# Kernel optimization log

Hardware: AMD Instinct MI355X
Metric: run time of the kernel (lower is better)

Reference implementation:

```python
import jax, jax.numpy as jnp
import numpy as np
from math import sqrt

DIM = 256
NUM_HEADS = 4
GROUPS = 32  # min(256//4, 32)
EPS = 1e-6


def group_norm(x, gamma, beta, groups=GROUPS, eps=EPS):
    # x: (B, C, H, W); normalize per group over (C//G, H, W)
    B, C, H, W = x.shape
    xg = x.reshape(B, groups, C // groups, H, W)
    mu = jnp.mean(xg, axis=(2, 3, 4), keepdims=True)
    var = jnp.var(xg, axis=(2, 3, 4), keepdims=True)
    xn = ((xg - mu) * jax.lax.rsqrt(var + eps)).reshape(B, C, H, W)
    return xn * gamma[None, :, None, None] + beta[None, :, None, None]


def lin_on_channel(x, W, bias):
    # torch Linear on channel dim: W is (out, in)
    return jnp.einsum('bchw,oc->bohw', x, W) + bias[None, :, None, None]


def setup_inputs() -> dict:
    key = jax.random.key(0)
    ks = jax.random.split(key, 14)
    B, C, H, W = 16, DIM, 32, 32
    s = 1.0 / sqrt(DIM)
    return {
        'a': jax.random.normal(ks[0], (B, C, H, W), jnp.float32),
        'b': jax.random.normal(ks[1], (B, C, H, W), jnp.float32),
        'Wq': jax.random.normal(ks[2], (DIM, DIM), jnp.float32) * s,
        'bq': jnp.zeros((DIM,), jnp.float32),
        'Wk': jax.random.normal(ks[3], (DIM, DIM), jnp.float32) * s,
        'bk': jnp.zeros((DIM,), jnp.float32),
        'Wv': jax.random.normal(ks[4], (DIM, DIM), jnp.float32) * s,
        'bv': jnp.zeros((DIM,), jnp.float32),
        'Wp': jax.random.normal(ks[5], (DIM, DIM), jnp.float32) * s,
        'bp': jnp.zeros((DIM,), jnp.float32),
        'gnA_w': jnp.ones((DIM,), jnp.float32),
        'gnA_b': jnp.zeros((DIM,), jnp.float32),
        'gnB_w': jnp.ones((DIM,), jnp.float32),
        'gnB_b': jnp.zeros((DIM,), jnp.float32),
    }


def reference(a, b, Wq, bq, Wk, bk, Wv, bv, Wp, bp, gnA_w, gnA_b, gnB_w, gnB_b):
    B, C, H, W = a.shape
    _, _, H2, W2 = b.shape
    dh = DIM // NUM_HEADS
    skip_b = b
    an = group_norm(a, gnA_w, gnA_b)
    bn = group_norm(b, gnB_w, gnB_b)
    q = lin_on_channel(bn, Wq, bq).reshape(B, NUM_HEADS, dh, H2, W2)
    k = lin_on_channel(an, Wk, bk).reshape(B, NUM_HEADS, dh, H, W)
    # NOTE: value uses pre-posemb but post-groupnorm 'a' (same as an here)
    v = lin_on_channel(an, Wv, bv).reshape(B, NUM_HEADS, dh, H, W)
    scores = jnp.einsum('bhdxy,bhdij->bhxyij', q, k) / sqrt(DIM)
    attn = jax.nn.softmax(scores.reshape(B, NUM_HEADS, H2, W2, H * W), axis=-1)
    attn = attn.reshape(B, NUM_HEADS, H2, W2, H, W)
    h = jnp.einsum('bhxyij,bhdij->bhdxy', attn, v).reshape(B, DIM, H2, W2)
    h = lin_on_channel(h, Wp, bp)
    ret = skip_b + h
    return ret / sqrt(2.0)
```

## Files before the change

kernel.cpp:

```cpp
#include <hip/hip_runtime.h>
#include <hip/hip_bf16.h>

#define BSZ 16
#define CDIM 256
#define NPIX 1024
#define NH 4
#define DHD 64
#define EPSV 1e-6f
#define QSCALE 0.0625f
#define INV_SQRT2 0.70710678118654752440f

typedef __attribute__((ext_vector_type(4))) float f32x4;
typedef __attribute__((ext_vector_type(8))) __bf16 bf16x8;
typedef __attribute__((ext_vector_type(4))) __bf16 bf16x4;

#define ASYNC16(gp, lp) __builtin_amdgcn_global_load_lds( \
    (const __attribute__((address_space(1))) void*)(gp),  \
    (__attribute__((address_space(3))) void*)(lp), 16, 0, 0)

#define OFF_WBF   0UL
#define OFF_STATS (512UL*1024)
#define OFF_ANT   (1024UL*1024)
#define OFF_BNT   (OFF_ANT + 8UL*1024*1024)
#define OFF_Q     (OFF_BNT + 8UL*1024*1024)
#define OFF_K     (OFF_Q   + 8UL*1024*1024)
#define OFF_V     (OFF_K   + 8UL*1024*1024)
#define OFF_H     (OFF_V   + 8UL*1024*1024)

__global__ __launch_bounds__(256) void prep_w(const float* __restrict__ Wq, const float* __restrict__ Wk,
                                              const float* __restrict__ Wv, const float* __restrict__ Wp,
                                              __bf16* __restrict__ out){
  int m = blockIdx.y;
  const float* src = (m==0)?Wq:(m==1)?Wk:(m==2)?Wv:Wp;
  float scale = (m==0)?QSCALE:1.0f;
  int idx = (blockIdx.x*256 + threadIdx.x)*4;
  float4 v = *(const float4*)(src + idx);
  bf16x4 o;
  o[0]=(__bf16)(v.x*scale); o[1]=(__bf16)(v.y*scale);
  o[2]=(__bf16)(v.z*scale); o[3]=(__bf16)(v.w*scale);
  *(bf16x4*)(out + m*65536 + idx) = o;
}

__global__ __launch_bounds__(256) void gn_stats(const float* __restrict__ xa, const float* __restrict__ xb,
                                                float2* __restrict__ stats){
  int bx = blockIdx.x;
  int t = bx >> 9; int rem = bx & 511; int bb = rem >> 5; int g = rem & 31;
  const float* src = (t ? xb : xa) + ((size_t)(bb*CDIM + g*8))*NPIX;
  float s = 0.f, ss = 0.f;
  for (int i = 0; i < 8; i++){
    float4 v = *(const float4*)(src + (threadIdx.x + 256*i)*4);
    s  += v.x+v.y+v.z+v.w;
    ss += v.x*v.x+v.y*v.y+v.z*v.z+v.w*v.w;
  }
  __shared__ float rs[256], rss[256];
  rs[threadIdx.x]=s; rss[threadIdx.x]=ss; __syncthreads();
  for (int st=128; st>0; st>>=1){
    if (threadIdx.x < st){ rs[threadIdx.x]+=rs[threadIdx.x+st]; rss[threadIdx.x]+=rss[threadIdx.x+st]; }
    __syncthreads();
  }
  if (threadIdx.x==0){
    float mean = rs[0]*(1.0f/8192.0f);
    float var  = rss[0]*(1.0f/8192.0f) - mean*mean;
    stats[(t*16+bb)*32+g] = make_float2(mean, rsqrtf(var + EPSV));
  }
}

__global__ __launch_bounds__(256) void norm_t(const float* __restrict__ xa, const float* __restrict__ xb,
                                              const float* __restrict__ gAw, const float* __restrict__ gAb,
                                              const float* __restrict__ gBw, const float* __restrict__ gBb,
                                              const float2* __restrict__ stats,
                                              __bf16* __restrict__ ant, __bf16* __restrict__ bnt){
  __shared__ __align__(16) __bf16 T[64][72];
  int t = blockIdx.z;
  const float* src = t ? xb : xa;
  const float* gw  = t ? gBw : gAw;
  const float* gb  = t ? gBb : gAb;
  __bf16* dst = t ? bnt : ant;
  int bb = blockIdx.y >> 2, cblk = blockIdx.y & 3;
  int p0 = blockIdx.x*64, c0 = cblk*64;
  int tid = threadIdx.x;
  int r16 = tid>>4, c4 = tid&15;
  for (int pass=0; pass<4; pass++){
    int cl = r16 + 16*pass;
    int c  = c0 + cl;
    float2 ms = stats[(t*16+bb)*32 + (c>>3)];
    float sc  = ms.y * gw[c];
    float off = gb[c] - ms.x*sc;
    float4 v = *(const float4*)(src + ((size_t)(bb*CDIM + c))*NPIX + p0 + c4*4);
    T[c4*4+0][cl] = (__bf16)(v.x*sc+off);
    T[c4*4+1][cl] = (__bf16)(v.y*sc+off);
    T[c4*4+2][cl] = (__bf16)(v.z*sc+off);
    T[c4*4+3][cl] = (__bf16)(v.w*sc+off);
  }
  __syncthreads();
  for (int pass=0; pass<2; pass++){
    int slot = tid + 256*pass;
    int pl = slot>>3, ch = slot&7;
    *(float4*)(dst + ((size_t)(bb*NPIX + p0 + pl))*CDIM + c0 + ch*8) = *(float4*)&T[pl][ch*8];
  }
}

__global__ __launch_bounds__(256,2) void gemm_qk(const __bf16* __restrict__ Wqk,
    const __bf16* __restrict__ bnt, const __bf16* __restrict__ ant,
    const float* __restrict__ bq, const float* __restrict__ bk,
    __bf16* __restrict__ qws, __bf16* __restrict__ kws){
  __shared__ __align__(16) __bf16 As[128][76], Bs[128][76];
  int i0 = blockIdx.x;
  int wg = (i0&7)*64 + (i0>>3);
  int my = wg&3, nx = wg>>2;
  int m0 = my*128, n0 = nx*128;
  const __bf16* Bm = (my<2) ? bnt : ant;
  int tid=threadIdx.x, lane=tid&63, wid=tid>>6;
  int wm=(wid>>1)*64, wn=(wid&1)*64, g=lane>>4, c=lane&15;
  f32x4 acc[4][4];
  #pragma unroll
  for (int i=0;i<4;i++)
    #pragma unroll
    for (int j=0;j<4;j++) acc[i][j]=(f32x4){0.f,0.f,0.f,0.f};
  int row[4], ch[4];
  #pragma unroll
  for (int i=0;i<4;i++){ int slot=tid+256*i; row[i]=slot>>3; ch[i]=slot&7; }
  for (int k0=0; k0<256; k0+=64){
    #pragma unroll
    for (int i=0;i<4;i++){
      *(float4*)&As[row[i]][ch[i]*8] = *(const float4*)(Wqk + (size_t)(m0+row[i])*256 + k0 + ch[i]*8);
      *(float4*)&Bs[row[i]][ch[i]*8] = *(const float4*)(Bm  + (size_t)(n0+row[i])*256 + k0 + ch[i]*8);
    }
    __syncthreads();
    #pragma unroll
    for (int ks=0;ks<2;ks++){
      bf16x8 af[4], bfr[4];
      #pragma unroll
      for (int i=0;i<4;i++) af[i]  = *(bf16x8*)&As[wm+i*16+c][ks*32+g*8];
      #pragma unroll
      for (int j=0;j<4;j++) bfr[j] = *(bf16x8*)&Bs[wn+j*16+c][ks*32+g*8];
      #pragma unroll
      for (int i=0;i<4;i++)
        #pragma unroll
        for (int j=0;j<4;j++)
          acc[i][j] = __builtin_amdgcn_mfma_f32_16x16x32_bf16(af[i], bfr[j], acc[i][j],0,0,0);
    }
    __syncthreads();
  }
  const float* bias = (my<2)? bq : bk;
  float bscale = (my<2)? QSCALE : 1.0f;
  __bf16* dst = (my<2)? qws : kws;
  int mbase = (my<2)? m0 : (m0-256);
  #pragma unroll
  for (int fm=0;fm<4;fm++){
    #pragma unroll
    for (int fn=0;fn<4;fn++){
      int o = mbase + wm + fm*16 + g*4;
      int n = n0 + wn + fn*16 + c;
      int bb=n>>10, p=n&1023;
      f32x4 v = acc[fm][fn];
      bf16x4 pk;
      #pragma unroll
      for (int r=0;r<4;r++) pk[r] = (__bf16)(v[r] + bias[o+r]*bscale);
      *(bf16x4*)(dst + ((size_t)((bb*4+(o>>6))*1024 + p))*64 + (o&63)) = pk;
    }
  }
}

__global__ __launch_bounds__(256,2) void gemm_sw(const __bf16* __restrict__ A,
    const __bf16* __restrict__ Wn, const float* __restrict__ bias,
    void* __restrict__ dst_, const float* __restrict__ skip, int mode){
  __shared__ __align__(16) __bf16 As[128][76], Bs[64][76];
  int i0 = blockIdx.x;
  int wg = (i0&7)*64 + (i0>>3);
  int ny = wg&3, mx = wg>>2;
  int m0 = mx*128, n0 = ny*64;
  int tid=threadIdx.x, lane=tid&63, wid=tid>>6;
  int wm=(wid>>1)*64, wn=(wid&1)*32, g=lane>>4, c=lane&15;
  f32x4 acc[4][2];
  #pragma unroll
  for (int i=0;i<4;i++)
    #pragma unroll
    for (int j=0;j<2;j++) acc[i][j]=(f32x4){0.f,0.f,0.f,0.f};
  int rowA[4], chA[4], rowB[2], chB[2];
  #pragma unroll
  for (int i=0;i<4;i++){ int slot=tid+256*i; rowA[i]=slot>>3; chA[i]=slot&7; }
  #pragma unroll
  for (int i=0;i<2;i++){ int slot=tid+256*i; rowB[i]=slot>>3; chB[i]=slot&7; }
  for (int k0=0; k0<256; k0+=64){
    #pragma unroll
    for (int i=0;i<4;i++)
      *(float4*)&As[rowA[i]][chA[i]*8] = *(const float4*)(A  + (size_t)(m0+rowA[i])*256 + k0 + chA[i]*8);
    #pragma unroll
    for (int i=0;i<2;i++)
      *(float4*)&Bs[rowB[i]][chB[i]*8] = *(const float4*)(Wn + (size_t)(n0+rowB[i])*256 + k0 + chB[i]*8);
    __syncthreads();
    #pragma unroll
    for (int ks=0;ks<2;ks++){
      bf16x8 af[4], bfr[2];
      #pragma unroll
      for (int i=0;i<4;i++) af[i]  = *(bf16x8*)&As[wm+i*16+c][ks*32+g*8];
      #pragma unroll
      for (int j=0;j<2;j++) bfr[j] = *(bf16x8*)&Bs[wn+j*16+c][ks*32+g*8];
      #pragma unroll
      for (int i=0;i<4;i++)
        #pragma unroll
        for (int j=0;j<2;j++)
          acc[i][j] = __builtin_amdgcn_mfma_f32_16x16x32_bf16(af[i], bfr[j], acc[i][j],0,0,0);
    }
    __syncthreads();
  }
  #pragma unroll
  for (int fm=0;fm<4;fm++){
    #pragma unroll
    for (int fn=0;fn<2;fn++){
      int m = m0 + wm + fm*16 + g*4;
      int n = n0 + wn + fn*16 + c;
      int bb=m>>10, p=m&1023;
      f32x4 v = acc[fm][fn];
      if (mode==0){
        float bv = bias[n];
        bf16x4 pk;
        #pragma unroll
        for (int r=0;r<4;r++) pk[r] = (__bf16)(v[r] + bv);
        *(bf16x4*)((__bf16*)dst_ + ((size_t)((bb*4+(n>>6))*64 + (n&63)))*1024 + p) = pk;
      } else {
        float bv = bias[n];
        size_t addr = (size_t)(bb*256 + n)*1024 + p;
        float4 sk = *(const float4*)(skip + addr);
        float4 ov;
        ov.x=(sk.x+v[0]+bv)*INV_SQRT2; ov.y=(sk.y+v[1]+bv)*INV_SQRT2;
        ov.z=(sk.z+v[2]+bv)*INV_SQRT2; ov.w=(sk.w+v[3]+bv)*INV_SQRT2;
        *(float4*)((float*)dst_ + addr) = ov;
      }
    }
  }
}

__global__ __launch_bounds__(256,4) void attn_k(const __bf16* __restrict__ q, const __bf16* __restrict__ k,
                                                const __bf16* __restrict__ v, __bf16* __restrict__ hout){
  __shared__ __align__(16) __bf16 Kb[2][4096];
  __shared__ __align__(16) __bf16 Vb[2][4096];
  __shared__ __align__(16) __bf16 Pl[4][1024];
  int i0 = blockIdx.x;
  int wg = (i0&7)*128 + (i0>>3);
  int bh = wg>>4, qblk = wg&15;
  int tid = threadIdx.x, lane = tid&63, w = tid>>6;
  int g = lane>>4, c = lane&15;
  int bb = bh>>2, h = bh&3;
  const char* kbyte = (const char*)(k + (size_t)bh*NPIX*DHD);
  const char* vbyte = (const char*)(v + (size_t)bh*DHD*NPIX);
  const __bf16* qbase = q + (size_t)bh*NPIX*DHD;

  int qrow = qblk*64 + w*16 + c;
  bf16x8 qf0 = *(const bf16x8*)(qbase + (size_t)qrow*64 +      g*8);
  bf16x8 qf1 = *(const bf16x8*)(qbase + (size_t)qrow*64 + 32 + g*8);

  int srow = w*8 + (lane>>3);
  int scol = ((lane&7) ^ (lane>>3)) << 4;
  const char* ks0 = kbyte + srow*128 + scol;
  const char* vs0 = vbyte + (size_t)srow*2048 + scol;

  f32x4 oacc[4];
  #pragma unroll
  for (int i=0;i<4;i++) oacc[i] = (f32x4){0.f,0.f,0.f,0.f};
  float la0=0.f, la1=0.f, la2=0.f, la3=0.f;
  int cs = (c&7)<<4;
  char* pw = (char*)&Pl[w][0];

  #define STAGE(buf, kt) { \
    const char* ks_ = ks0 + (size_t)(kt)*8192; \
    const char* vs_ = vs0 + (size_t)(kt)*128; \
    ASYNC16(ks_,          &Kb[buf][w*512]); \
    ASYNC16(ks_ + 4096,   &Kb[buf][2048 + w*512]); \
    ASYNC16(vs_,          &Vb[buf][w*512]); \
    ASYNC16(vs_ + 65536,  &Vb[buf][2048 + w*512]); }

  STAGE(0, 0)
  for (int kt=0; kt<16; kt++){
    int cur = kt&1;
    __syncthreads();
    if (kt<15) STAGE(cur^1, kt+1)
    const char* KL = (const char*)&Kb[cur][0];
    const char* VL = (const char*)&Vb[cur][0];
    f32x4 s[4];
    #pragma unroll
    for (int fn=0; fn<4; fn++){
      int r = fn*16+c;
      bf16x8 kb0 = *(const bf16x8*)(KL + r*128 + ((     g*16) ^ cs));
      bf16x8 kb1 = *(const bf16x8*)(KL + r*128 + ((64 + g*16) ^ cs));
      f32x4 z = (f32x4){0.f,0.f,0.f,0.f};
      z     = __builtin_amdgcn_mfma_f32_16x16x32_bf16(qf0, kb0, z, 0,0,0);
      s[fn] = __builtin_amdgcn_mfma_f32_16x16x32_bf16(qf1, kb1, z, 0,0,0);
    }
    #pragma unroll
    for (int fn=0; fn<4; fn++){
      int cb = (fn*16+c)*2;
      float p0 = __expf(s[fn][0]); la0 += p0;
      float p1 = __expf(s[fn][1]); la1 += p1;
      float p2 = __expf(s[fn][2]); la2 += p2;
      float p3 = __expf(s[fn][3]); la3 += p3;
      *(__bf16*)(pw + (g*4+0)*128 + (cb ^ (((g*4+0)&7)<<4))) = (__bf16)p0;
      *(__bf16*)(pw + (g*4+1)*128 + (cb ^ (((g*4+1)&7)<<4))) = (__bf16)p1;
      *(__bf16*)(pw + (g*4+2)*128 + (cb ^ (((g*4+2)&7)<<4))) = (__bf16)p2;
      *(__bf16*)(pw + (g*4+3)*128 + (cb ^ (((g*4+3)&7)<<4))) = (__bf16)p3;
    }
    bf16x8 pb0 = *(const bf16x8*)(pw + c*128 + ((     g*16) ^ cs));
    bf16x8 pb1 = *(const bf16x8*)(pw + c*128 + ((64 + g*16) ^ cs));
    #pragma unroll
    for (int fm=0; fm<4; fm++){
      int r = fm*16+c;
      bf16x8 va0 = *(const bf16x8*)(VL + r*128 + ((     g*16) ^ cs));
      bf16x8 va1 = *(const bf16x8*)(VL + r*128 + ((64 + g*16) ^ cs));
      oacc[fm] = __builtin_amdgcn_mfma_f32_16x16x32_bf16(va0, pb0, oacc[fm], 0,0,0);
      oacc[fm] = __builtin_amdgcn_mfma_f32_16x16x32_bf16(va1, pb1, oacc[fm], 0,0,0);
    }
  }
  #undef STAGE

  la0 += __shfl_xor(la0,1); la0 += __shfl_xor(la0,2); la0 += __shfl_xor(la0,4); la0 += __shfl_xor(la0,8);
  la1 += __shfl_xor(la1,1); la1 += __shfl_xor(la1,2); la1 += __shfl_xor(la1,4); la1 += __shfl_xor(la1,8);
  la2 += __shfl_xor(la2,1); la2 += __shfl_xor(la2,2); la2 += __shfl_xor(la2,4); la2 += __shfl_xor(la2,8);
  la3 += __shfl_xor(la3,1); la3 += __shfl_xor(la3,2); la3 += __shfl_xor(la3,4); la3 += __shfl_xor(la3,8);
  float vsel = ((c&3)==0)? la0 : ((c&3)==1)? la1 : ((c&3)==2)? la2 : la3;
  float lq = __shfl(vsel, (c>>2)*16 + (c&3));
  float linv = 1.0f / lq;

  int qg = qblk*64 + w*16 + c;
  #pragma unroll
  for (int fm=0; fm<4; fm++){
    bf16x4 pk;
    #pragma unroll
    for (int r=0;r<4;r++) pk[r] = (__bf16)(oacc[fm][r]*linv);
    *(bf16x4*)(hout + ((size_t)(bb*NPIX + qg))*CDIM + h*64 + fm*16 + g*4) = pk;
  }
}

extern "C" void kernel_launch(void* const* d_in, const int* in_sizes, int n_in,
                              void* d_out, int out_size, void* d_ws, size_t ws_size,
                              hipStream_t stream) {
  const float* xa  = (const float*)d_in[0];
  const float* xb  = (const float*)d_in[1];
  const float* Wq  = (const float*)d_in[2];
  const float* bq  = (const float*)d_in[3];
  const float* Wk  = (const float*)d_in[4];
  const float* bk  = (const float*)d_in[5];
  const float* Wv  = (const float*)d_in[6];
  const float* bv  = (const float*)d_in[7];
  const float* Wp  = (const float*)d_in[8];
  const float* bp  = (const float*)d_in[9];
  const float* gAw = (const float*)d_in[10];
  const float* gAb = (const float*)d_in[11];
  const float* gBw = (const float*)d_in[12];
  const float* gBb = (const float*)d_in[13];

  char* ws = (char*)d_ws;
  __bf16* wbf   = (__bf16*)(ws + OFF_WBF);
  float2* stats = (float2*)(ws + OFF_STATS);
  __bf16* ant   = (__bf16*)(ws + OFF_ANT);
  __bf16* bnt   = (__bf16*)(ws + OFF_BNT);
  __bf16* qws   = (__bf16*)(ws + OFF_Q);
  __bf16* kws   = (__bf16*)(ws + OFF_K);
  __bf16* vws   = (__bf16*)(ws + OFF_V);
  __bf16* hws   = (__bf16*)(ws + OFF_H);

  prep_w<<<dim3(64,4), 256, 0, stream>>>(Wq, Wk, Wv, Wp, wbf);
  gn_stats<<<1024, 256, 0, stream>>>(xa, xb, stats);
  norm_t<<<dim3(16,64,2), 256, 0, stream>>>(xa, xb, gAw, gAb, gBw, gBb, stats, ant, bnt);
  gemm_qk<<<512, 256, 0, stream>>>(wbf, bnt, ant, bq, bk, qws, kws);
  gemm_sw<<<512, 256, 0, stream>>>(ant, wbf + 2*65536, bv, vws, nullptr, 0);
  attn_k<<<1024, 256, 0, stream>>>(qws, kws, vws, hws);
  gemm_sw<<<512, 256, 0, stream>>>(hws, wbf + 3*65536, bp, d_out, xb, 1);
}
```

Measured before the change: 174.5 us.

## Fuse group-norm stats with normalize-transpose and merge QK and V projection launches

```diff
diff --git a/kernel.cpp b/kernel.cpp
--- a/kernel.cpp
+++ b/kernel.cpp
@@ -41,123 +41,167 @@
   *(bf16x4*)(out + m*65536 + idx) = o;
 }
 
-__global__ __launch_bounds__(256) void gn_stats(const float* __restrict__ xa, const float* __restrict__ xb,
-                                                float2* __restrict__ stats){
+__global__ __launch_bounds__(256) void gn_fused(const float* __restrict__ xa, const float* __restrict__ xb,
+    const float* __restrict__ gAw, const float* __restrict__ gAb,
+    const float* __restrict__ gBw, const float* __restrict__ gBb,
+    __bf16* __restrict__ ant, __bf16* __restrict__ bnt){
+  __shared__ float S[8192];
+  __shared__ float red[8];
   int bx = blockIdx.x;
-  int t = bx >> 9; int rem = bx & 511; int bb = rem >> 5; int g = rem & 31;
-  const float* src = (t ? xb : xa) + ((size_t)(bb*CDIM + g*8))*NPIX;
-  float s = 0.f, ss = 0.f;
-  for (int i = 0; i < 8; i++){
-    float4 v = *(const float4*)(src + (threadIdx.x + 256*i)*4);
+  int t = bx>>9, rem = bx&511, b = rem>>5, g = rem&31;
+  const float* src = (t ? xb : xa) + ((size_t)(b*CDIM + g*8))*NPIX;
+  const float* gw  = t ? gBw : gAw;
+  const float* gb  = t ? gBb : gAb;
+  __bf16* dst = (t ? bnt : ant) + (size_t)b*NPIX*CDIM + g*8;
+  int tid = threadIdx.x, lane = tid&63, w = tid>>6;
+  float s=0.f, ss=0.f;
+  #pragma unroll
+  for (int k=0;k<8;k++){
+    int flat = tid + 256*k;
+    float4 v = *(const float4*)(src + (size_t)flat*4);
+    *(float4*)&S[flat*4] = v;
     s  += v.x+v.y+v.z+v.w;
     ss += v.x*v.x+v.y*v.y+v.z*v.z+v.w*v.w;
   }
-  __shared__ float rs[256], rss[256];
-  rs[threadIdx.x]=s; rss[threadIdx.x]=ss; __syncthreads();
-  for (int st=128; st>0; st>>=1){
-    if (threadIdx.x < st){ rs[threadIdx.x]+=rs[threadIdx.x+st]; rss[threadIdx.x]+=rss[threadIdx.x+st]; }
-    __syncthreads();
-  }
-  if (threadIdx.x==0){
-    float mean = rs[0]*(1.0f/8192.0f);
-    float var  = rss[0]*(1.0f/8192.0f) - mean*mean;
-    stats[(t*16+bb)*32+g] = make_float2(mean, rsqrtf(var + EPSV));
-  }
-}
-
-__global__ __launch_bounds__(256) void norm_t(const float* __restrict__ xa, const float* __restrict__ xb,
-                                              const float* __restrict__ gAw, const float* __restrict__ gAb,
-                                              const float* __restrict__ gBw, const float* __restrict__ gBb,
-                                              const float2* __restrict__ stats,
-                                              __bf16* __restrict__ ant, __bf16* __restrict__ bnt){
-  __shared__ __align__(16) __bf16 T[64][72];
-  int t = blockIdx.z;
-  const float* src = t ? xb : xa;
-  const float* gw  = t ? gBw : gAw;
-  const float* gb  = t ? gBb : gAb;
-  __bf16* dst = t ? bnt : ant;
-  int bb = blockIdx.y >> 2, cblk = blockIdx.y & 3;
-  int p0 = blockIdx.x*64, c0 = cblk*64;
-  int tid = threadIdx.x;
-  int r16 = tid>>4, c4 = tid&15;
-  for (int pass=0; pass<4; pass++){
-    int cl = r16 + 16*pass;
-    int c  = c0 + cl;
-    float2 ms = stats[(t*16+bb)*32 + (c>>3)];
-    float sc  = ms.y * gw[c];
-    float off = gb[c] - ms.x*sc;
-    float4 v = *(const float4*)(src + ((size_t)(bb*CDIM + c))*NPIX + p0 + c4*4);
-    T[c4*4+0][cl] = (__bf16)(v.x*sc+off);
-    T[c4*4+1][cl] = (__bf16)(v.y*sc+off);
-    T[c4*4+2][cl] = (__bf16)(v.z*sc+off);
-    T[c4*4+3][cl] = (__bf16)(v.w*sc+off);
-  }
+  #pragma unroll
+  for (int m=32;m>0;m>>=1){ s += __shfl_xor(s,m); ss += __shfl_xor(ss,m); }
+  if (lane==0){ red[w]=s; red[4+w]=ss; }
   __syncthreads();
-  for (int pass=0; pass<2; pass++){
-    int slot = tid + 256*pass;
-    int pl = slot>>3, ch = slot&7;
-    *(float4*)(dst + ((size_t)(bb*NPIX + p0 + pl))*CDIM + c0 + ch*8) = *(float4*)&T[pl][ch*8];
-  }
-}
-
-__global__ __launch_bounds__(256,2) void gemm_qk(const __bf16* __restrict__ Wqk,
+  float st  = red[0]+red[1]+red[2]+red[3];
+  float sst = red[4]+red[5]+red[6]+red[7];
+  float mean = st*(1.0f/8192.0f);
+  float var  = sst*(1.0f/8192.0f) - mean*mean;
+  float rstd = rsqrtf(var + EPSV);
+  float sc[8], off[8];
+  #pragma unroll
+  for (int c2=0;c2<8;c2++){ sc[c2]=rstd*gw[g*8+c2]; off[c2]=gb[g*8+c2]-mean*sc[c2]; }
+  #pragma unroll
+  for (int k=0;k<4;k++){
+    int px = tid + 256*k;
+    bf16x8 o;
+    #pragma unroll
+    for (int c2=0;c2<8;c2++) o[c2] = (__bf16)(S[c2*1024+px]*sc[c2]+off[c2]);
+    *(bf16x8*)(dst + (size_t)px*CDIM) = o;
+  }
+}
+
+__global__ __launch_bounds__(256,2) void gemm_qkv(const __bf16* __restrict__ Wqk,
     const __bf16* __restrict__ bnt, const __bf16* __restrict__ ant,
     const float* __restrict__ bq, const float* __restrict__ bk,
-    __bf16* __restrict__ qws, __bf16* __restrict__ kws){
+    __bf16* __restrict__ qws, __bf16* __restrict__ kws,
+    const __bf16* __restrict__ Wv, const float* __restrict__ bv,
+    __bf16* __restrict__ vws){
   __shared__ __align__(16) __bf16 As[128][76], Bs[128][76];
-  int i0 = blockIdx.x;
-  int wg = (i0&7)*64 + (i0>>3);
-  int my = wg&3, nx = wg>>2;
-  int m0 = my*128, n0 = nx*128;
-  const __bf16* Bm = (my<2) ? bnt : ant;
   int tid=threadIdx.x, lane=tid&63, wid=tid>>6;
-  int wm=(wid>>1)*64, wn=(wid&1)*64, g=lane>>4, c=lane&15;
-  f32x4 acc[4][4];
-  #pragma unroll
-  for (int i=0;i<4;i++)
-    #pragma unroll
-    for (int j=0;j<4;j++) acc[i][j]=(f32x4){0.f,0.f,0.f,0.f};
-  int row[4], ch[4];
-  #pragma unroll
-  for (int i=0;i<4;i++){ int slot=tid+256*i; row[i]=slot>>3; ch[i]=slot&7; }
-  for (int k0=0; k0<256; k0+=64){
-    #pragma unroll
-    for (int i=0;i<4;i++){
-      *(float4*)&As[row[i]][ch[i]*8] = *(const float4*)(Wqk + (size_t)(m0+row[i])*256 + k0 + ch[i]*8);
-      *(float4*)&Bs[row[i]][ch[i]*8] = *(const float4*)(Bm  + (size_t)(n0+row[i])*256 + k0 + ch[i]*8);
-    }
-    __syncthreads();
-    #pragma unroll
-    for (int ks=0;ks<2;ks++){
-      bf16x8 af[4], bfr[4];
-      #pragma unroll
-      for (int i=0;i<4;i++) af[i]  = *(bf16x8*)&As[wm+i*16+c][ks*32+g*8];
-      #pragma unroll
-      for (int j=0;j<4;j++) bfr[j] = *(bf16x8*)&Bs[wn+j*16+c][ks*32+g*8];
+  int g=lane>>4, c=lane&15;
+  if (blockIdx.x < 512){
+    int i0 = blockIdx.x;
+    int wg = (i0&7)*64 + (i0>>3);
+    int my = wg&3, nx = wg>>2;
+    int m0 = my*128, n0 = nx*128;
+    const __bf16* Bm = (my<2) ? bnt : ant;
+    int wm=(wid>>1)*64, wn=(wid&1)*64;
+    f32x4 acc[4][4];
+    #pragma unroll
+    for (int i=0;i<4;i++)
+      #pragma unroll
+      for (int j=0;j<4;j++) acc[i][j]=(f32x4){0.f,0.f,0.f,0.f};
+    int row[4], ch[4];
+    #pragma unroll
+    for (int i=0;i<4;i++){ int slot=tid+256*i; row[i]=slot>>3; ch[i]=slot&7; }
+    for (int k0=0; k0<256; k0+=64){
+      #pragma unroll
+      for (int i=0;i<4;i++){
+        *(float4*)&As[row[i]][ch[i]*8] = *(const float4*)(Wqk + (size_t)(m0+row[i])*256 + k0 + ch[i]*8);
+        *(float4*)&Bs[row[i]][ch[i]*8] = *(const float4*)(Bm  + (size_t)(n0+row[i])*256 + k0 + ch[i]*8);
+      }
+      __syncthreads();
+      #pragma unroll
+      for (int ks=0;ks<2;ks++){
+        bf16x8 af[4], bfr[4];
+        #pragma unroll
+        for (int i=0;i<4;i++) af[i]  = *(bf16x8*)&As[wm+i*16+c][ks*32+g*8];
+        #pragma unroll
+        for (int j=0;j<4;j++) bfr[j] = *(bf16x8*)&Bs[wn+j*16+c][ks*32+g*8];
+        #pragma unroll
+        for (int i=0;i<4;i++)
+          #pragma unroll
+          for (int j=0;j<4;j++)
+            acc[i][j] = __builtin_amdgcn_mfma_f32_16x16x32_bf16(af[i], bfr[j], acc[i][j],0,0,0);
+      }
+      __syncthreads();
+    }
+    const float* bias = (my<2)? bq : bk;
+    float bscale = (my<2)? QSCALE : 1.0f;
+    __bf16* dst = (my<2)? qws : kws;
+    int mbase = (my<2)? m0 : (m0-256);
+    #pragma unroll
+    for (int fm=0;fm<4;fm++){
+      #pragma unroll
+      for (int fn=0;fn<4;fn++){
+        int o = mbase + wm + fm*16 + g*4;
+        int n = n0 + wn + fn*16 + c;
+        int bb=n>>10, p=n&1023;
+        f32x4 v = acc[fm][fn];
+        bf16x4 pk;
+        #pragma unroll
+        for (int r=0;r<4;r++) pk[r] = (__bf16)(v[r] + bias[o+r]*bscale);
+        *(bf16x4*)(dst + ((size_t)((bb*4+(o>>6))*1024 + p))*64 + (o&63)) = pk;
+      }
+    }
+  } else {
+    int i0 = blockIdx.x - 512;
+    int wg = (i0&7)*64 + (i0>>3);
+    int ny = wg&3, mx = wg>>2;
+    int m0 = mx*128, n0 = ny*64;
+    int wm=(wid>>1)*64, wn=(wid&1)*32;
+    f32x4 acc[4][2];
+    #pragma unroll
+    for (int i=0;i<4;i++)
+      #pragma unroll
+      for (int j=0;j<2;j++) acc[i][j]=(f32x4){0.f,0.f,0.f,0.f};
+    int rowA[4], chA[4], rowB[2], chB[2];
+    #pragma unroll
+    for (int i=0;i<4;i++){ int slot=tid+256*i; rowA[i]=slot>>3; chA[i]=slot&7; }
+    #pragma unroll
+    for (int i=0;i<2;i++){ int slot=tid+256*i; rowB[i]=slot>>3; chB[i]=slot&7; }
+    for (int k0=0; k0<256; k0+=64){
       #pragma unroll
       for (int i=0;i<4;i++)
-        #pragma unroll
-        for (int j=0;j<4;j++)
-          acc[i][j] = __builtin_amdgcn_mfma_f32_16x16x32_bf16(af[i], bfr[j], acc[i][j],0,0,0);
-    }
-    __syncthreads();
-  }
-  const float* bias = (my<2)? bq : bk;
-  float bscale = (my<2)? QSCALE : 1.0f;
-  __bf16* dst = (my<2)? qws : kws;
-  int mbase = (my<2)? m0 : (m0-256);
-  #pragma unroll
-  for (int fm=0;fm<4;fm++){
-    #pragma unroll
-    for (int fn=0;fn<4;fn++){
-      int o = mbase + wm + fm*16 + g*4;
-      int n = n0 + wn + fn*16 + c;
-      int bb=n>>10, p=n&1023;
-      f32x4 v = acc[fm][fn];
-      bf16x4 pk;
-      #pragma unroll
-      for (int r=0;r<4;r++) pk[r] = (__bf16)(v[r] + bias[o+r]*bscale);
-      *(bf16x4*)(dst + ((size_t)((bb*4+(o>>6))*1024 + p))*64 + (o&63)) = pk;
+        *(float4*)&As[rowA[i]][chA[i]*8] = *(const float4*)(ant + (size_t)(m0+rowA[i])*256 + k0 + chA[i]*8);
+      #pragma unroll
+      for (int i=0;i<2;i++)
+        *(float4*)&Bs[rowB[i]][chB[i]*8] = *(const float4*)(Wv  + (size_t)(n0+rowB[i])*256 + k0 + chB[i]*8);
+      __syncthreads();
+      #pragma unroll
+      for (int ks=0;ks<2;ks++){
+        bf16x8 af[4], bfr[2];
+        #pragma unroll
+        for (int i=0;i<4;i++) af[i]  = *(bf16x8*)&As[wm+i*16+c][ks*32+g*8];
+        #pragma unroll
+        for (int j=0;j<2;j++) bfr[j] = *(bf16x8*)&Bs[wn+j*16+c][ks*32+g*8];
+        #pragma unroll
+        for (int i=0;i<4;i++)
+          #pragma unroll
+          for (int j=0;j<2;j++)
+            acc[i][j] = __builtin_amdgcn_mfma_f32_16x16x32_bf16(af[i], bfr[j], acc[i][j],0,0,0);
+      }
+      __syncthreads();
+    }
+    #pragma unroll
+    for (int fm=0;fm<4;fm++){
+      #pragma unroll
+      for (int fn=0;fn<2;fn++){
+        int m = m0 + wm + fm*16 + g*4;
+        int n = n0 + wn + fn*16 + c;
+        int bb=m>>10, p=m&1023;
+        f32x4 v = acc[fm][fn];
+        float bvv = bv[n];
+        bf16x4 pk;
+        #pragma unroll
+        for (int r=0;r<4;r++) pk[r] = (__bf16)(v[r] + bvv);
+        *(bf16x4*)(vws + ((size_t)((bb*4+(n>>6))*64 + (n&63)))*1024 + p) = pk;
+      }
     }
   }
 }
@@ -214,18 +258,18 @@
       int bb=m>>10, p=m&1023;
       f32x4 v = acc[fm][fn];
       if (mode==0){
-        float bv = bias[n];
+        float bvv = bias[n];
         bf16x4 pk;
         #pragma unroll
-        for (int r=0;r<4;r++) pk[r] = (__bf16)(v[r] + bv);
+        for (int r=0;r<4;r++) pk[r] = (__bf16)(v[r] + bvv);
         *(bf16x4*)((__bf16*)dst_ + ((size_t)((bb*4+(n>>6))*64 + (n&63)))*1024 + p) = pk;
       } else {
-        float bv = bias[n];
+        float bvv = bias[n];
         size_t addr = (size_t)(bb*256 + n)*1024 + p;
         float4 sk = *(const float4*)(skip + addr);
         float4 ov;
-        ov.x=(sk.x+v[0]+bv)*INV_SQRT2; ov.y=(sk.y+v[1]+bv)*INV_SQRT2;
-        ov.z=(sk.z+v[2]+bv)*INV_SQRT2; ov.w=(sk.w+v[3]+bv)*INV_SQRT2;
+        ov.x=(sk.x+v[0]+bvv)*INV_SQRT2; ov.y=(sk.y+v[1]+bvv)*INV_SQRT2;
+        ov.z=(sk.z+v[2]+bvv)*INV_SQRT2; ov.w=(sk.w+v[3]+bvv)*INV_SQRT2;
         *(float4*)((float*)dst_ + addr) = ov;
       }
     }
@@ -351,7 +395,6 @@
 
   char* ws = (char*)d_ws;
   __bf16* wbf   = (__bf16*)(ws + OFF_WBF);
-  float2* stats = (float2*)(ws + OFF_STATS);
   __bf16* ant   = (__bf16*)(ws + OFF_ANT);
   __bf16* bnt   = (__bf16*)(ws + OFF_BNT);
   __bf16* qws   = (__bf16*)(ws + OFF_Q);
@@ -360,10 +403,9 @@
   __bf16* hws   = (__bf16*)(ws + OFF_H);
 
   prep_w<<<dim3(64,4), 256, 0, stream>>>(Wq, Wk, Wv, Wp, wbf);
-  gn_stats<<<1024, 256, 0, stream>>>(xa, xb, stats);
-  norm_t<<<dim3(16,64,2), 256, 0, stream>>>(xa, xb, gAw, gAb, gBw, gBb, stats, ant, bnt);
-  gemm_qk<<<512, 256, 0, stream>>>(wbf, bnt, ant, bq, bk, qws, kws);
-  gemm_sw<<<512, 256, 0, stream>>>(ant, wbf + 2*65536, bv, vws, nullptr, 0);
+  gn_fused<<<1024, 256, 0, stream>>>(xa, xb, gAw, gAb, gBw, gBb, ant, bnt);
+  gemm_qkv<<<1024, 256, 0, stream>>>(wbf, bnt, ant, bq, bk, qws, kws,
+                                     wbf + 2*65536, bv, vws);
   attn_k<<<1024, 256, 0, stream>>>(qws, kws, vws, hws);
   gemm_sw<<<512, 256, 0, stream>>>(hws, wbf + 3*65536, bp, d_out, xb, 1);
 }
```

Result: no change. 171.8 us (-1.6%).
